# Optimization experiments

Hardware: AMD Instinct MI355X
Metric: run time of the kernel (lower is better)

The kernel has to match this reference:

```python
import jax, jax.numpy as jnp
import numpy as np

B, S, IN, E, L, H, NC, NL = 4, 1000, 5, 256, 6, 8, 2, 50
DH = E // H


def _ln(x, g, b, eps=1e-5):
    m = jnp.mean(x, -1, keepdims=True)
    v = jnp.mean((x - m) ** 2, -1, keepdims=True)
    return (x - m) / jnp.sqrt(v + eps) * g + b


def _lin(x, w, b):
    return x @ w.T + b


def _ph_single(points, fw, db, law, lab):
    # points: (S, 2) -> (6,) persistence features
    scores = (points @ law.T + lab)[:, 0]
    wts = jax.nn.softmax(scores)
    _, idx = jax.lax.top_k(wts, NL)
    lm = points[idx]  # (NL, 2) landmarks
    d2 = jnp.sum((lm[:, None, :] - lm[None, :, :]) ** 2, -1)
    # safe sqrt (zero grad on zero diagonal) == torch.cdist
    dist = jnp.sqrt(jnp.where(d2 > 0, d2, 1.0)) * (d2 > 0)
    sd = dist * jnp.abs(fw[0, 0]) + db[0]
    K = jnp.exp(-sd)
    lap = jnp.diag(jnp.sum(K, 1)) - K
    ev, evec = jnp.linalg.eigh(lap)
    zm = (ev < 1e-6).astype(ev.dtype)
    n0 = jnp.sum(zm)
    s0 = jnp.sum(jnp.abs(ev) * zm)
    gap = ev[1] - ev[0]
    fied = jnp.std(evec[:, 1], ddof=1)  # torch.std is unbiased
    return jnp.stack([n0, s0, gap, fied, jnp.mean(ev[2:6]), jnp.std(ev[2:6], ddof=1)])


def _attn(x, pf, qw, qb, kw, kb, vw, vb, pw1, pb1, pw2, pb2, ow_, ob_):
    b, s, e = x.shape
    q = _lin(x, qw, qb).reshape(b, s, H, DH).transpose(0, 2, 1, 3)
    k = _lin(x, kw, kb).reshape(b, s, H, DH).transpose(0, 2, 1, 3)
    v = _lin(x, vw, vb).reshape(b, s, H, DH).transpose(0, 2, 1, 3)
    scores = jnp.einsum('bhqd,bhkd->bhqk', q, k) / DH ** 0.5
    tw = jax.nn.sigmoid(_lin(jax.nn.relu(_lin(pf, pw1, pb1)), pw2, pb2))  # (b, E)
    # expand + mean over embed dim collapses to one scalar per sample
    ts = jnp.mean(tw, -1).reshape(b, 1, 1, 1)
    aw = jax.nn.softmax(scores * ts, -1)
    out = jnp.einsum('bhqk,bhkd->bhqd', aw, v).transpose(0, 2, 1, 3).reshape(b, s, e)
    return _lin(out, ow_, ob_)


def _fwd(sequences, ph_fw, ph_db, ph_law, ph_lab,
         emb_w1, emb_b1, emb_w2, emb_b2, emb_ln_g, emb_ln_b, pos_enc,
         qw, qb, kw, kb, vw, vb, pe_w1, pe_b1, pe_w2, pe_b2, ow, ob,
         ln_g, ln_b, f_w1, f_b1, f_w2, f_b2,
         c_ln_g, c_ln_b, c_w1, c_b1, c_w2, c_b2):
    b, s, _ = sequences.shape
    t = jnp.broadcast_to(jnp.arange(s, dtype=sequences.dtype), (b, s))
    pc = jnp.stack([t, jnp.mean(sequences, 2)], 2)  # (b, s, 2) point clouds
    pf = jax.vmap(lambda p: _ph_single(p, ph_fw, ph_db, ph_law, ph_lab))(pc)  # (b, 6)
    x = _ln(_lin(jax.nn.relu(_lin(sequences, emb_w1, emb_b1)), emb_w2, emb_b2),
            emb_ln_g, emb_ln_b)
    x = x + pos_enc[:s][None]
    for l in range(L):
        att = _attn(x, pf, qw[l], qb[l], kw[l], kb[l], vw[l], vb[l],
                    pe_w1[l], pe_b1[l], pe_w2[l], pe_b2[l], ow[l], ob[l])
        x = _ln(x + att, ln_g[l], ln_b[l])  # NOTE: same LN reused twice, as in source
        ff = _lin(jax.nn.gelu(_lin(x, f_w1[l], f_b1[l]), approximate=False), f_w2[l], f_b2[l])
        x = _ln(x + ff, ln_g[l], ln_b[l])
    pwts = jax.nn.softmax(jnp.sum(x, -1), -1)[..., None]
    pooled = jnp.sum(x * pwts, 1)
    z = jax.nn.relu(_lin(_ln(pooled, c_ln_g, c_ln_b), c_w1, c_b1))
    return _lin(z, c_w2, c_b2)


def setup_inputs() -> dict:
    key = jax.random.key(0)
    ks = iter(jax.random.split(key, 64))

    def w(shape, fan_in):
        return jax.random.normal(next(ks), shape, jnp.float32) / np.sqrt(fan_in).astype(np.float32)

    z = lambda *sh: jnp.zeros(sh, jnp.float32)
    o = lambda *sh: jnp.ones(sh, jnp.float32)
    return dict(
        sequences=jax.random.normal(next(ks), (B, S, IN), jnp.float32),
        ph_fw=jnp.full((1, 1), 0.02, jnp.float32),  # small filtration scale keeps eigh well-conditioned
        ph_db=z(1),
        ph_law=w((1, 2), 2), ph_lab=z(1),
        emb_w1=w((E // 2, IN), IN), emb_b1=z(E // 2),
        emb_w2=w((E, E // 2), E // 2), emb_b2=z(E),
        emb_ln_g=o(E), emb_ln_b=z(E),
        pos_enc=jax.random.normal(next(ks), (1000, E), jnp.float32),
        qw=w((L, E, E), E), qb=z(L, E),
        kw=w((L, E, E), E), kb=z(L, E),
        vw=w((L, E, E), E), vb=z(L, E),
        pe_w1=w((L, E // 2, 6), 6), pe_b1=z(L, E // 2),
        pe_w2=w((L, E, E // 2), E // 2), pe_b2=z(L, E),
        ow=w((L, E, E), E), ob=z(L, E),
        ln_g=o(L, E), ln_b=z(L, E),
        f_w1=w((L, 4 * E, E), E), f_b1=z(L, 4 * E),
        f_w2=w((L, E, 4 * E), 4 * E), f_b2=z(L, E),
        c_ln_g=o(E), c_ln_b=z(E),
        c_w1=w((E // 2, E), E), c_b1=z(E // 2),
        c_w2=w((NC, E // 2), E // 2), c_b2=z(NC),
    )


def reference(sequences, ph_fw, ph_db, ph_law, ph_lab,
              emb_w1, emb_b1, emb_w2, emb_b2, emb_ln_g, emb_ln_b, pos_enc,
              qw, qb, kw, kb, vw, vb, pe_w1, pe_b1, pe_w2, pe_b2, ow, ob,
              ln_g, ln_b, f_w1, f_b1, f_w2, f_b2,
              c_ln_g, c_ln_b, c_w1, c_b1, c_w2, c_b2):
    return _fwd(sequences, ph_fw, ph_db, ph_law, ph_lab,
                emb_w1, emb_b1, emb_w2, emb_b2, emb_ln_g, emb_ln_b, pos_enc,
                qw, qb, kw, kb, vw, vb, pe_w1, pe_b1, pe_w2, pe_b2, ow, ob,
                ln_g, ln_b, f_w1, f_b1, f_w2, f_b2,
                c_ln_g, c_ln_b, c_w1, c_b1, c_w2, c_b2)
```

## Files before the change

kernel.cpp:

```cpp
#include <hip/hip_runtime.h>
#include <math.h>

constexpr int BB = 4;
constexpr int SS = 1000;
constexpr int INDIM = 5;
constexpr int EE = 256;
constexpr int LL = 6;
constexpr int HH = 8;
constexpr int DHH = 32;
constexpr int NLM = 50;
constexpr int FFD = 1024;

typedef short short8 __attribute__((ext_vector_type(8)));
typedef float f32x4 __attribute__((ext_vector_type(4)));
typedef unsigned short u16;
typedef unsigned long long u64;

__device__ inline u16 f2b(float f) {
  union { float f; unsigned u; } v; v.f = f;
  unsigned u = v.u;
  unsigned r = u + 0x7FFFu + ((u >> 16) & 1u);
  return (u16)(r >> 16);
}
__device__ inline float b2f(u16 b) {
  union { unsigned u; float f; } v; v.u = ((unsigned)b) << 16;
  return v.f;
}
__device__ inline short8 pack8(float4 a, float4 b) {
  short8 r;
  r[0] = (short)f2b(a.x); r[1] = (short)f2b(a.y);
  r[2] = (short)f2b(a.z); r[3] = (short)f2b(a.w);
  r[4] = (short)f2b(b.x); r[5] = (short)f2b(b.y);
  r[6] = (short)f2b(b.z); r[7] = (short)f2b(b.w);
  return r;
}

__device__ inline double wred_sum(double v) {
#pragma unroll
  for (int m = 1; m < 64; m <<= 1) v += __shfl_xor(v, m, 64);
  return v;
}
__device__ inline double wred_min(double v) {
#pragma unroll
  for (int m = 1; m < 64; m <<= 1) v = fmin(v, __shfl_xor(v, m, 64));
  return v;
}
__device__ inline double wred_max(double v) {
#pragma unroll
  for (int m = 1; m < 64; m <<= 1) v = fmax(v, __shfl_xor(v, m, 64));
  return v;
}
__device__ inline float wredf_sum(float v) {
#pragma unroll
  for (int m = 1; m < 64; m <<= 1) v += __shfl_xor(v, m, 64);
  return v;
}
__device__ inline int sgnbit(double x) {
  return (int)((unsigned long long)__double_as_longlong(x) >> 63);
}

struct PhS {
  double matA[NLM][51];
  union {
    u64 keys[1024];
    double vstore[NLM - 2][64];
  } u;
  double vbuf[64], wbuf[64];
  double pm[4][64];
  double dar[NLM], ear[NLM], e2a[NLM], tauA[NLM], evs[NLM];
  double gdl[NLM], gdd[NLM], gdu[NLM], gdu2[NLM], gz[NLM];
  float sm[SS];
  float lx[NLM], ly[NLM];
};
union FusedS { PhS ph; float h[4][128]; };

__global__ __launch_bounds__(256) void phembed_kernel(
    const float* __restrict__ seq, const float* __restrict__ ph_fw,
    const float* __restrict__ ph_db, const float* __restrict__ ph_law,
    const float* __restrict__ ph_lab, float* __restrict__ pf,
    const float* __restrict__ ew1, const float* __restrict__ eb1,
    const float* __restrict__ ew2, const float* __restrict__ eb2,
    const float* __restrict__ eg, const float* __restrict__ ebe,
    const float* __restrict__ pos, float* __restrict__ X)
{
  __shared__ FusedS S;
  const int tid = threadIdx.x;
  const int lane = tid & 63, wid = tid >> 6;

  if (blockIdx.x < BB) {
    const int b = blockIdx.x;
    PhS& P = S.ph;
    const float law0 = ph_law[0], law1 = ph_law[1], labv = ph_lab[0];
    for (int s = tid; s < 1024; s += 256) {
      u64 key;
      if (s < SS) {
        const float* p = seq + ((size_t)b * SS + s) * INDIM;
        float m = (p[0] + p[1] + p[2] + p[3] + p[4]) * 0.2f;
        P.sm[s] = m;
        float sc = (float)s * law0 + m * law1 + labv;
        unsigned u = __float_as_uint(sc);
        unsigned asc = (u & 0x80000000u) ? ~u : (u | 0x80000000u);
        key = ((u64)(~asc) << 32) | (unsigned)s;
      } else {
        key = (0xFFFFFFFFull << 32) | (unsigned)s;
      }
      P.u.keys[s] = key;
    }
    __syncthreads();
    for (int k = 2; k <= 1024; k <<= 1) {
      for (int j = k >> 1; j > 0; j >>= 1) {
        for (int i = tid; i < 1024; i += 256) {
          int ixj = i ^ j;
          if (ixj > i) {
            u64 a = P.u.keys[i], c = P.u.keys[ixj];
            bool up = ((i & k) == 0);
            if ((a > c) == up) { P.u.keys[i] = c; P.u.keys[ixj] = a; }
          }
        }
        __syncthreads();
      }
    }
    if (tid < NLM) {
      int id = (int)(P.u.keys[tid] & 0xFFFFFFFFull);
      P.lx[tid] = (float)id;
      P.ly[tid] = P.sm[id];
    }
    __syncthreads();
    const float fwv = fabsf(ph_fw[0]);
    const float dbv = ph_db[0];
    for (int t = tid; t < NLM * NLM; t += 256) {
      int i = t / NLM, j = t % NLM;
      float dx = P.lx[i] - P.lx[j], dy = P.ly[i] - P.ly[j];
      float d2 = dx * dx + dy * dy;
      float dist = (d2 > 0.f) ? sqrtf(d2) : 0.f;
      float Kv = expf(-(dist * fwv + dbv));
      P.matA[i][j] = -(double)Kv;
    }
    __syncthreads();
    if (tid < NLM) {
      double rsum = 0.0;
      for (int j = 0; j < NLM; ++j) rsum -= P.matA[tid][j];
      P.matA[tid][tid] += rsum;
    }
    __syncthreads();

    for (int k = 0; k <= NLM - 3; ++k) {
      if (wid == 0) {
        double x = (lane > k && lane < NLM) ? P.matA[lane][k] : 0.0;
        double x0 = __shfl(x, k + 1, 64);
        double sigma = wred_sum((lane > k + 1) ? x * x : 0.0);
        double beta, tau, scale;
        if (sigma == 0.0) { beta = x0; tau = 0.0; scale = 0.0; }
        else {
          double nrm = sqrt(x0 * x0 + sigma);
          beta = (x0 >= 0.0) ? -nrm : nrm;
          tau = (beta - x0) / beta;
          scale = 1.0 / (x0 - beta);
        }
        double v = (lane == k + 1) ? 1.0 : ((lane > k + 1 && lane < NLM) ? x * scale : 0.0);
        P.vbuf[lane] = v;
        P.u.vstore[k][lane] = v;
        if (lane == 0) { P.ear[k] = beta; P.tauA[k] = tau; }
      }
      __syncthreads();
      {
        double partial = 0.0;
        if (lane < NLM) {
          int j0 = wid * 13;
#pragma unroll
          for (int jj = 0; jj < 13; ++jj) {
            int j = j0 + jj;
            if (j < NLM) partial += P.matA[lane][j] * P.vbuf[j];
          }
        }
        P.pm[wid][lane] = partial;
      }
      __syncthreads();
      if (wid == 0) {
        double tau = P.tauA[k];
        double p = 0.0;
        if (lane < NLM)
          p = (P.pm[0][lane] + P.pm[1][lane] + P.pm[2][lane] + P.pm[3][lane]) * tau;
        double vr = P.vbuf[lane];
        double dotvp = wred_sum(vr * p);
        double w = p - 0.5 * tau * dotvp * vr;
        P.wbuf[lane] = (lane < NLM) ? w : 0.0;
      }
      __syncthreads();
      if (lane < NLM) {
        double vr = P.vbuf[lane], wr = P.wbuf[lane];
        int j0 = wid * 13;
#pragma unroll
        for (int jj = 0; jj < 13; ++jj) {
          int j = j0 + jj;
          if (j < NLM) P.matA[lane][j] -= vr * P.wbuf[j] + wr * P.vbuf[j];
        }
      }
      __syncthreads();
    }
    if (tid < NLM) P.dar[tid] = P.matA[tid][tid];
    if (tid == 0) P.ear[NLM - 2] = P.matA[NLM - 1][NLM - 2];
    __syncthreads();
    if (tid < NLM - 1) P.e2a[tid] = P.ear[tid] * P.ear[tid];
    __syncthreads();

    double lo_i = 1e300, hi_i = -1e300;
    if (lane < NLM) {
      double rl = (lane > 0) ? fabs(P.ear[lane - 1]) : 0.0;
      double rr = (lane < NLM - 1) ? fabs(P.ear[lane]) : 0.0;
      double dd = P.dar[lane];
      lo_i = dd - rl - rr;
      hi_i = dd + rl + rr;
    }
    double glo = wred_min(lo_i), ghi = wred_max(hi_i);

    if (tid < 100) {
      const int e = tid >> 1;
      const int side = tid & 1;
      const int need = e + 1;
      double lo = glo, hi = ghi;
      for (int it = 0; it < 24; ++it) {
        double third = (hi - lo) * (1.0 / 3.0);
        double x1 = lo + third, x2 = hi - third;
        double x = side ? x2 : x1;
        double p = P.dar[0] - x, q = 1.0;
        int c = sgnbit(p);
#pragma unroll 7
        for (int i = 1; i < NLM; ++i) {
          double n = (P.dar[i] - x) * p - P.e2a[i - 1] * q;
          if (n == 0.0) n = sgnbit(p) ? -1e-300 : 1e-300;
          c += (sgnbit(n) != sgnbit(p));
          long long an = __double_as_longlong(n) & 0x7fffffffffffffffLL;
          long long ap = __double_as_longlong(p) & 0x7fffffffffffffffLL;
          int E = (int)((an > ap ? an : ap) >> 52);
          int se = 2046 - E; se = se < 1 ? 1 : (se > 2045 ? 2045 : se);
          double s = __longlong_as_double((long long)se << 52);
          q = p * s; p = n * s;
        }
        int cp = __shfl_xor(c, 1, 64);
        int c1 = side ? cp : c;
        int c2 = side ? c : cp;
        if (c1 >= need) hi = x1;
        else if (c2 >= need) { lo = x1; hi = x2; }
        else lo = x2;
      }
      if (side == 0) P.evs[e] = 0.5 * (lo + hi);
    }
    __syncthreads();

    if (wid != 0) return;

    if (lane == 0) {
      double shift = P.evs[1];
      unsigned rs = 12345u;
      for (int i = 0; i < NLM; ++i) {
        rs = rs * 1103515245u + 12345u;
        P.gz[i] = ((double)((rs >> 8) & 0xFFFF)) / 65536.0 - 0.5;
      }
      for (int iter = 0; iter < 2; ++iter) {
        for (int i = 0; i < NLM; ++i) P.gdd[i] = P.dar[i] - shift;
        for (int i = 0; i < NLM - 1; ++i) { P.gdl[i] = P.ear[i]; P.gdu[i] = P.ear[i]; }
        for (int i = 0; i < NLM - 1; ++i) {
          if (fabs(P.gdd[i]) >= fabs(P.gdl[i])) {
            if (P.gdd[i] == 0.0) P.gdd[i] = 1e-280;
            double fact = P.gdl[i] / P.gdd[i];
            P.gdd[i + 1] -= fact * P.gdu[i];
            P.gz[i + 1] -= fact * P.gz[i];
            if (i < NLM - 2) P.gdu2[i] = 0.0;
          } else {
            double fact = P.gdd[i] / P.gdl[i];
            P.gdd[i] = P.gdl[i];
            double tmp = P.gdd[i + 1];
            P.gdd[i + 1] = P.gdu[i] - fact * tmp;
            if (i < NLM - 2) { P.gdu2[i] = P.gdu[i + 1]; P.gdu[i + 1] = -fact * P.gdu2[i]; }
            P.gdu[i] = tmp;
            double tz = P.gz[i]; P.gz[i] = P.gz[i + 1]; P.gz[i + 1] = tz - fact * P.gz[i];
          }
        }
        if (P.gdd[NLM - 1] == 0.0) P.gdd[NLM - 1] = 1e-280;
        P.gz[NLM - 1] /= P.gdd[NLM - 1];
        P.gz[NLM - 2] = (P.gz[NLM - 2] - P.gdu[NLM - 2] * P.gz[NLM - 1]) / P.gdd[NLM - 2];
        for (int i = NLM - 3; i >= 0; --i)
          P.gz[i] = (P.gz[i] - P.gdu[i] * P.gz[i + 1] - P.gdu2[i] * P.gz[i + 2]) / P.gdd[i];
        double nr = 0.0;
        for (int i = 0; i < NLM; ++i) nr += P.gz[i] * P.gz[i];
        nr = sqrt(nr);
        for (int i = 0; i < NLM; ++i) P.gz[i] /= nr;
      }
    }
    __builtin_amdgcn_wave_barrier();
    double fied = (lane < NLM) ? P.gz[lane] : 0.0;
    for (int k = NLM - 3; k >= 0; --k) {
      double v = P.u.vstore[k][lane];
      double dot = wred_sum(v * fied);
      fied -= P.tauA[k] * dot * v;
    }

    double myev = (lane < NLM) ? P.evs[lane] : 1e300;
    bool inR = (lane < NLM);
    double n0 = wred_sum((inR && myev < 1e-6) ? 1.0 : 0.0);
    double s0 = wred_sum((inR && myev < 1e-6) ? fabs(myev) : 0.0);
    double e0 = P.evs[0], e1 = P.evs[1];
    double e2 = P.evs[2], e3 = P.evs[3], e4 = P.evs[4], e5 = P.evs[5];
    double gap = e1 - e0;
    double m4 = (e2 + e3 + e4 + e5) * 0.25;
    double v4 = ((e2 - m4) * (e2 - m4) + (e3 - m4) * (e3 - m4) +
                 (e4 - m4) * (e4 - m4) + (e5 - m4) * (e5 - m4)) / 3.0;
    double fmean = wred_sum(inR ? fied : 0.0) / NLM;
    double fd = inR ? (fied - fmean) : 0.0;
    double fvar = wred_sum(fd * fd) / (NLM - 1);
    if (lane == 0) {
      float* o = pf + b * 6;
      o[0] = (float)n0;
      o[1] = (float)s0;
      o[2] = (float)gap;
      o[3] = (float)sqrt(fvar);
      o[4] = (float)m4;
      o[5] = (float)sqrt(v4);
    }
    return;
  }

  const int row = (blockIdx.x - BB) * 4 + wid;
  const int s = row % SS;
  float* hb = S.h[wid];
  float sv0, sv1, sv2, sv3, sv4;
  {
    const float* p = seq + (size_t)row * INDIM;
    sv0 = p[0]; sv1 = p[1]; sv2 = p[2]; sv3 = p[3]; sv4 = p[4];
  }
#pragma unroll
  for (int half = 0; half < 2; ++half) {
    int j = lane + half * 64;
    const float* w = ew1 + j * INDIM;
    float a = eb1[j] + w[0] * sv0 + w[1] * sv1 + w[2] * sv2 + w[3] * sv3 + w[4] * sv4;
    hb[j] = fmaxf(a, 0.f);
  }
  __builtin_amdgcn_wave_barrier();
  float o4[4];
#pragma unroll
  for (int q = 0; q < 4; ++q) {
    int e = lane * 4 + q;
    const float* w = ew2 + (size_t)e * 128;
    float a0 = 0.f, a1 = 0.f;
    for (int i = 0; i < 128; i += 8) {
      float4 wa = *(const float4*)(w + i);
      float4 wb = *(const float4*)(w + i + 4);
      a0 += wa.x * hb[i] + wa.y * hb[i + 1] + wa.z * hb[i + 2] + wa.w * hb[i + 3];
      a1 += wb.x * hb[i + 4] + wb.y * hb[i + 5] + wb.z * hb[i + 6] + wb.w * hb[i + 7];
    }
    o4[q] = eb2[e] + a0 + a1;
  }
  float ssum = o4[0] + o4[1] + o4[2] + o4[3];
  ssum = wredf_sum(ssum);
  float mean = ssum * (1.f / EE);
  float d0 = o4[0] - mean, d1 = o4[1] - mean, d2 = o4[2] - mean, d3 = o4[3] - mean;
  float qsum = d0 * d0 + d1 * d1 + d2 * d2 + d3 * d3;
  qsum = wredf_sum(qsum);
  float inv = rsqrtf(qsum * (1.f / EE) + 1e-5f);
  float4 gv = *(const float4*)(eg + lane * 4);
  float4 bv = *(const float4*)(ebe + lane * 4);
  float4 pv = *(const float4*)(pos + (size_t)s * EE + lane * 4);
  float4 outv = make_float4(d0 * inv * gv.x + bv.x + pv.x,
                            d1 * inv * gv.y + bv.y + pv.y,
                            d2 * inv * gv.z + bv.z + pv.z,
                            d3 * inv * gv.w + bv.w + pv.w);
  *(float4*)(X + (size_t)row * EE + lane * 4) = outv;
}

__global__ __launch_bounds__(256) void temp_kernel(
    const float* __restrict__ pf, const float* __restrict__ w1, const float* __restrict__ b1,
    const float* __restrict__ w2, const float* __restrict__ b2, float* __restrict__ ts)
{
  const int l = blockIdx.x / BB, b = blockIdx.x % BB, tid = threadIdx.x;
  __shared__ float pfl[6];
  __shared__ float h[128];
  __shared__ float red[256];
  if (tid < 6) pfl[tid] = pf[b * 6 + tid];
  __syncthreads();
  if (tid < 128) {
    const float* w = w1 + ((size_t)l * 128 + tid) * 6;
    float a = b1[(size_t)l * 128 + tid];
#pragma unroll
    for (int i = 0; i < 6; ++i) a += w[i] * pfl[i];
    h[tid] = fmaxf(a, 0.f);
  }
  __syncthreads();
  const float* w = w2 + ((size_t)l * EE + tid) * 128;
  float a = b2[(size_t)l * EE + tid];
  for (int i = 0; i < 128; ++i) a += w[i] * h[i];
  float sg = 1.f / (1.f + expf(-a));
  red[tid] = sg; __syncthreads();
  for (int wd = 128; wd > 0; wd >>= 1) { if (tid < wd) red[tid] += red[tid + wd]; __syncthreads(); }
  if (tid == 0) ts[l * BB + b] = red[0] * (1.f / EE);
}

template <int AF32, int ACT>
__global__ __launch_bounds__(256) void gemm_bt(
    const void* __restrict__ Aptr,
    const float* __restrict__ W0, const float* __restrict__ W1, const float* __restrict__ W2,
    const float* __restrict__ bb0, const float* __restrict__ bb1, const float* __restrict__ bb2,
    u16* __restrict__ C0, u16* __restrict__ C1, u16* __restrict__ C2,
    int M, int N, int K)
{
  const int z = blockIdx.z;
  const float* W = (z == 0) ? W0 : (z == 1) ? W1 : W2;
  const float* bias = (z == 0) ? bb0 : (z == 1) ? bb1 : bb2;
  u16* C = (z == 0) ? C0 : (z == 1) ? C1 : C2;
  __shared__ __align__(16) u16 As[2][64][40];
  __shared__ __align__(16) u16 Bs[2][64][40];
  const int m0 = blockIdx.x * 64, n0 = blockIdx.y * 64;
  const int tid = threadIdx.x;
  const int lane = tid & 63, wave = tid >> 6;
  const int wm = wave >> 1, wn = wave & 1;
  const int l15 = lane & 15, l4 = lane >> 4;
  const int srow = tid >> 2, scg = (tid & 3) * 8;

  const float* Af = (const float*)Aptr;
  const u16* Ab = (const u16*)Aptr;

  f32x4 acc[2][2];
#pragma unroll
  for (int i = 0; i < 2; ++i)
#pragma unroll
    for (int j = 0; j < 2; ++j) acc[i][j] = (f32x4){0.f, 0.f, 0.f, 0.f};

  short8 areg, breg;
  auto do_load = [&](int t) {
    int kk = t * 32 + scg;
    if (AF32) {
      float4 a0 = *(const float4*)(Af + (size_t)(m0 + srow) * K + kk);
      float4 a1 = *(const float4*)(Af + (size_t)(m0 + srow) * K + kk + 4);
      areg = pack8(a0, a1);
    } else {
      areg = *(const short8*)(Ab + (size_t)(m0 + srow) * K + kk);
    }
    float4 b0 = *(const float4*)(W + (size_t)(n0 + srow) * K + kk);
    float4 b1 = *(const float4*)(W + (size_t)(n0 + srow) * K + kk + 4);
    breg = pack8(b0, b1);
  };
  auto do_write = [&](int buf) {
    *(short8*)&As[buf][srow][scg] = areg;
    *(short8*)&Bs[buf][srow][scg] = breg;
  };

  const int NT = K / 32;
  do_load(0);
  do_write(0);
  __syncthreads();
  for (int t = 0; t < NT; ++t) {
    const int cur = t & 1;
    if (t + 1 < NT) do_load(t + 1);
    short8 af0 = *(const short8*)&As[cur][wm * 32 + l15][l4 * 8];
    short8 af1 = *(const short8*)&As[cur][wm * 32 + 16 + l15][l4 * 8];
    short8 bf0 = *(const short8*)&Bs[cur][wn * 32 + l15][l4 * 8];
    short8 bf1 = *(const short8*)&Bs[cur][wn * 32 + 16 + l15][l4 * 8];
    acc[0][0] = __builtin_amdgcn_mfma_f32_16x16x32_bf16(af0, bf0, acc[0][0], 0, 0, 0);
    acc[0][1] = __builtin_amdgcn_mfma_f32_16x16x32_bf16(af0, bf1, acc[0][1], 0, 0, 0);
    acc[1][0] = __builtin_amdgcn_mfma_f32_16x16x32_bf16(af1, bf0, acc[1][0], 0, 0, 0);
    acc[1][1] = __builtin_amdgcn_mfma_f32_16x16x32_bf16(af1, bf1, acc[1][1], 0, 0, 0);
    if (t + 1 < NT) do_write(cur ^ 1);
    __syncthreads();
  }
#pragma unroll
  for (int nf = 0; nf < 2; ++nf) {
    int col = n0 + wn * 32 + nf * 16 + l15;
    float bv = bias[col];
#pragma unroll
    for (int mf = 0; mf < 2; ++mf) {
#pragma unroll
      for (int r = 0; r < 4; ++r) {
        int row = m0 + wm * 32 + mf * 16 + l4 * 4 + r;
        if (row < M) {
          float v = acc[mf][nf][r] + bv;
          if (ACT == 1) v = 0.5f * v * (1.f + erff(v * 0.70710678118654752440f));
          C[(size_t)row * N + col] = f2b(v);
        }
      }
    }
  }
}

__global__ __launch_bounds__(256) void attn_mfma(
    const u16* __restrict__ Qm, const u16* __restrict__ Km, const u16* __restrict__ Vm,
    const float* __restrict__ ts, u16* __restrict__ Om, int l)
{
  const int qt = blockIdx.x, h = blockIdx.y, b = blockIdx.z;
  const int tid = threadIdx.x;
  const int lane = tid & 63, wave = tid >> 6;
  const int l15 = lane & 15, l4 = lane >> 4;
  const float scale = ts[l * BB + b] * 0.17677669529663688110f;
  __shared__ __align__(16) u16 Ks[64][40];
  __shared__ __align__(16) u16 Vt[32][72];
  __shared__ __align__(16) u16 Pw[4][16][72];
  const int q0 = qt * 64 + wave * 16;
  const int srow = tid >> 2, scg = (tid & 3) * 8;

  short8 qf = {0, 0, 0, 0, 0, 0, 0, 0};
  {
    int qrow = q0 + l15;
    if (qrow < SS)
      qf = *(const short8*)(Qm + ((size_t)(b * SS + qrow)) * EE + h * DHH + l4 * 8);
  }

  float mrun[4] = {-INFINITY, -INFINITY, -INFINITY, -INFINITY};
  float lrun[4] = {0.f, 0.f, 0.f, 0.f};
  f32x4 Oacc[2];
  Oacc[0] = (f32x4){0.f, 0.f, 0.f, 0.f};
  Oacc[1] = (f32x4){0.f, 0.f, 0.f, 0.f};

  for (int k0 = 0; k0 < SS; k0 += 64) {
    int kn = SS - k0; if (kn > 64) kn = 64;
    __syncthreads();
    {
      short8 kv8 = {0, 0, 0, 0, 0, 0, 0, 0};
      if (srow < kn)
        kv8 = *(const short8*)(Km + ((size_t)(b * SS + k0 + srow)) * EE + h * DHH + scg);
      *(short8*)&Ks[srow][scg] = kv8;
    }
    {
      int d = tid & 31, kb = tid >> 5;
      u16 uu[8];
#pragma unroll
      for (int i = 0; i < 8; ++i) {
        int kv = kb * 8 + i;
        uu[i] = (kv < kn) ? Vm[((size_t)(b * SS + k0 + kv)) * EE + h * DHH + d] : (u16)0;
      }
      *(ushort4*)(&Vt[d][kb * 8])     = make_ushort4(uu[0], uu[1], uu[2], uu[3]);
      *(ushort4*)(&Vt[d][kb * 8 + 4]) = make_ushort4(uu[4], uu[5], uu[6], uu[7]);
    }
    __syncthreads();

    f32x4 sa[4];
#pragma unroll
    for (int nf = 0; nf < 4; ++nf) {
      short8 kf = *(const short8*)(&Ks[nf * 16 + l15][l4 * 8]);
      f32x4 zz = (f32x4){0.f, 0.f, 0.f, 0.f};
      sa[nf] = __builtin_amdgcn_mfma_f32_16x16x32_bf16(qf, kf, zz, 0, 0, 0);
    }
#pragma unroll
    for (int nf = 0; nf < 4; ++nf) {
      bool valid = (nf * 16 + l15) < kn;
#pragma unroll
      for (int r = 0; r < 4; ++r)
        sa[nf][r] = valid ? sa[nf][r] * scale : -INFINITY;
    }
    float pv[4][4];
#pragma unroll
    for (int r = 0; r < 4; ++r) {
      float tmax = fmaxf(fmaxf(sa[0][r], sa[1][r]), fmaxf(sa[2][r], sa[3][r]));
#pragma unroll
      for (int m = 1; m < 16; m <<= 1) tmax = fmaxf(tmax, __shfl_xor(tmax, m, 64));
      float mnew = fmaxf(mrun[r], tmax);
      float fac = expf(mrun[r] - mnew);
      float rsum = 0.f;
#pragma unroll
      for (int nf = 0; nf < 4; ++nf) {
        float p = expf(sa[nf][r] - mnew);
        pv[nf][r] = p;
        rsum += p;
      }
#pragma unroll
      for (int m = 1; m < 16; m <<= 1) rsum += __shfl_xor(rsum, m, 64);
      lrun[r] = lrun[r] * fac + rsum;
      mrun[r] = mnew;
      Oacc[0][r] *= fac;
      Oacc[1][r] *= fac;
    }
#pragma unroll
    for (int nf = 0; nf < 4; ++nf)
#pragma unroll
      for (int r = 0; r < 4; ++r)
        Pw[wave][l4 * 4 + r][nf * 16 + l15] = f2b(pv[nf][r]);
    asm volatile("s_waitcnt lgkmcnt(0)" ::: "memory");
    __builtin_amdgcn_sched_barrier(0);
#pragma unroll
    for (int ka = 0; ka < 2; ++ka) {
      short8 pa = *(const short8*)(&Pw[wave][l15][ka * 32 + l4 * 8]);
#pragma unroll
      for (int df = 0; df < 2; ++df) {
        short8 vf = *(const short8*)(&Vt[df * 16 + l15][ka * 32 + l4 * 8]);
        Oacc[df] = __builtin_amdgcn_mfma_f32_16x16x32_bf16(pa, vf, Oacc[df], 0, 0, 0);
      }
    }
  }
#pragma unroll
  for (int df = 0; df < 2; ++df)
#pragma unroll
    for (int r = 0; r < 4; ++r) {
      int qrow = q0 + l4 * 4 + r;
      if (qrow < SS)
        Om[((size_t)(b * SS + qrow)) * EE + h * DHH + df * 16 + l15] = f2b(Oacc[df][r] / lrun[r]);
    }
}

__global__ __launch_bounds__(256) void addln_kernel(
    float* __restrict__ X, const u16* __restrict__ T,
    const float* __restrict__ g, const float* __restrict__ be)
{
  const int row = blockIdx.x * 4 + (threadIdx.x >> 6);
  const int lane = threadIdx.x & 63;
  float4 xv = *(float4*)(X + (size_t)row * EE + lane * 4);
  ushort4 tv = *(const ushort4*)(T + (size_t)row * EE + lane * 4);
  float4 v = make_float4(xv.x + b2f(tv.x), xv.y + b2f(tv.y),
                         xv.z + b2f(tv.z), xv.w + b2f(tv.w));
  float s = v.x + v.y + v.z + v.w;
  s = wredf_sum(s);
  float mean = s * (1.f / EE);
  float4 d = make_float4(v.x - mean, v.y - mean, v.z - mean, v.w - mean);
  float q = d.x * d.x + d.y * d.y + d.z * d.z + d.w * d.w;
  q = wredf_sum(q);
  float inv = rsqrtf(q * (1.f / EE) + 1e-5f);
  float4 gv = *(const float4*)(g + lane * 4);
  float4 bv = *(const float4*)(be + lane * 4);
  float4 o = make_float4(d.x * inv * gv.x + bv.x, d.y * inv * gv.y + bv.y,
                         d.z * inv * gv.z + bv.z, d.w * inv * gv.w + bv.w);
  *(float4*)(X + (size_t)row * EE + lane * 4) = o;
}

__global__ __launch_bounds__(256) void final_kernel(
    const float* __restrict__ X, const float* __restrict__ g, const float* __restrict__ be,
    const float* __restrict__ w1, const float* __restrict__ b1,
    const float* __restrict__ w2, const float* __restrict__ b2,
    float* __restrict__ out)
{
  const int b = blockIdx.x, tid = threadIdx.x;
  __shared__ float rs[SS];
  __shared__ float red[256];
  __shared__ float pooled[EE];
  __shared__ float h[128];
  for (int s = tid; s < SS; s += 256) {
    const float* xr = X + ((size_t)(b * SS + s)) * EE;
    float a = 0.f;
    for (int e = 0; e < EE; ++e) a += xr[e];
    rs[s] = a;
  }
  __syncthreads();
  float mx = -INFINITY;
  for (int s = tid; s < SS; s += 256) mx = fmaxf(mx, rs[s]);
  red[tid] = mx; __syncthreads();
  for (int w = 128; w > 0; w >>= 1) { if (tid < w) red[tid] = fmaxf(red[tid], red[tid + w]); __syncthreads(); }
  mx = red[0]; __syncthreads();
  float sme = 0.f;
  for (int s = tid; s < SS; s += 256) { float e2 = expf(rs[s] - mx); rs[s] = e2; sme += e2; }
  red[tid] = sme; __syncthreads();
  for (int w = 128; w > 0; w >>= 1) { if (tid < w) red[tid] += red[tid + w]; __syncthreads(); }
  float tot = red[0]; __syncthreads();
  float acc = 0.f;
  for (int s = 0; s < SS; ++s) acc += X[((size_t)(b * SS + s)) * EE + tid] * rs[s];
  acc /= tot;
  red[tid] = acc; __syncthreads();
  for (int w = 128; w > 0; w >>= 1) { if (tid < w) red[tid] += red[tid + w]; __syncthreads(); }
  float mean = red[0] * (1.f / EE); __syncthreads();
  float d = acc - mean;
  red[tid] = d * d; __syncthreads();
  for (int w = 128; w > 0; w >>= 1) { if (tid < w) red[tid] += red[tid + w]; __syncthreads(); }
  float var = red[0] * (1.f / EE);
  pooled[tid] = d * rsqrtf(var + 1e-5f) * g[tid] + be[tid];
  __syncthreads();
  if (tid < 128) {
    const float* w = w1 + (size_t)tid * EE;
    float a = b1[tid];
    for (int e = 0; e < EE; ++e) a += w[e] * pooled[e];
    h[tid] = fmaxf(a, 0.f);
  }
  __syncthreads();
  if (tid < 2) {
    const float* w = w2 + (size_t)tid * 128;
    float a = b2[tid];
    for (int j = 0; j < 128; ++j) a += w[j] * h[j];
    out[b * 2 + tid] = a;
  }
}

extern "C" void kernel_launch(void* const* d_in, const int* in_sizes, int n_in,
                              void* d_out, int out_size, void* d_ws, size_t ws_size,
                              hipStream_t stream) {
  (void)in_sizes; (void)n_in; (void)out_size; (void)ws_size;
  const float* seq    = (const float*)d_in[0];
  const float* ph_fw  = (const float*)d_in[1];
  const float* ph_db  = (const float*)d_in[2];
  const float* ph_law = (const float*)d_in[3];
  const float* ph_lab = (const float*)d_in[4];
  const float* emb_w1 = (const float*)d_in[5];
  const float* emb_b1 = (const float*)d_in[6];
  const float* emb_w2 = (const float*)d_in[7];
  const float* emb_b2 = (const float*)d_in[8];
  const float* eln_g  = (const float*)d_in[9];
  const float* eln_b  = (const float*)d_in[10];
  const float* pos    = (const float*)d_in[11];
  const float* qw     = (const float*)d_in[12];
  const float* qb     = (const float*)d_in[13];
  const float* kw     = (const float*)d_in[14];
  const float* kb     = (const float*)d_in[15];
  const float* vw     = (const float*)d_in[16];
  const float* vb     = (const float*)d_in[17];
  const float* pw1    = (const float*)d_in[18];
  const float* pb1    = (const float*)d_in[19];
  const float* pw2    = (const float*)d_in[20];
  const float* pb2    = (const float*)d_in[21];
  const float* ow     = (const float*)d_in[22];
  const float* obv    = (const float*)d_in[23];
  const float* lng    = (const float*)d_in[24];
  const float* lnb    = (const float*)d_in[25];
  const float* fw1    = (const float*)d_in[26];
  const float* fb1    = (const float*)d_in[27];
  const float* fw2    = (const float*)d_in[28];
  const float* fb2    = (const float*)d_in[29];
  const float* clng   = (const float*)d_in[30];
  const float* clnb   = (const float*)d_in[31];
  const float* cw1    = (const float*)d_in[32];
  const float* cb1    = (const float*)d_in[33];
  const float* cw2    = (const float*)d_in[34];
  const float* cb2    = (const float*)d_in[35];

  float* ws  = (float*)d_ws;
  float* pf  = ws;
  float* tsv = ws + 32;
  const size_t SL = (size_t)4096 * 256;
  float* X = ws + 256;
  u16* Qb   = (u16*)(X + SL);
  u16* Kb   = Qb + SL;
  u16* Vb   = Kb + SL;
  u16* ATTb = Vb + SL;
  u16* TMPb = ATTb + SL;
  u16* HIDb = TMPb + SL;
  const int M = BB * SS;

  phembed_kernel<<<BB + M / 4, 256, 0, stream>>>(
      seq, ph_fw, ph_db, ph_law, ph_lab, pf,
      emb_w1, emb_b1, emb_w2, emb_b2, eln_g, eln_b, pos, X);
  temp_kernel<<<LL * BB, 256, 0, stream>>>(pf, pw1, pb1, pw2, pb2, tsv);

  const int GM = 63;
  for (int l = 0; l < LL; ++l) {
    const size_t wo = (size_t)l * EE * EE;
    gemm_bt<1, 0><<<dim3(GM, EE / 64, 3), 256, 0, stream>>>(
        X, qw + wo, kw + wo, vw + wo, qb + l * EE, kb + l * EE, vb + l * EE,
        Qb, Kb, Vb, M, EE, EE);
    attn_mfma<<<dim3(16, HH, BB), 256, 0, stream>>>(Qb, Kb, Vb, tsv, ATTb, l);
    gemm_bt<0, 0><<<dim3(GM, EE / 64, 1), 256, 0, stream>>>(
        ATTb, ow + wo, ow + wo, ow + wo, obv + l * EE, obv + l * EE, obv + l * EE,
        TMPb, TMPb, TMPb, M, EE, EE);
    addln_kernel<<<M / 4, 256, 0, stream>>>(X, TMPb, lng + l * EE, lnb + l * EE);
    gemm_bt<1, 1><<<dim3(GM, FFD / 64, 1), 256, 0, stream>>>(
        X, fw1 + (size_t)l * FFD * EE, fw1 + (size_t)l * FFD * EE, fw1 + (size_t)l * FFD * EE,
        fb1 + (size_t)l * FFD, fb1 + (size_t)l * FFD, fb1 + (size_t)l * FFD,
        HIDb, HIDb, HIDb, M, FFD, EE);
    gemm_bt<0, 0><<<dim3(GM, EE / 64, 1), 256, 0, stream>>>(
        HIDb, fw2 + (size_t)l * EE * FFD, fw2 + (size_t)l * EE * FFD, fw2 + (size_t)l * EE * FFD,
        fb2 + l * EE, fb2 + l * EE, fb2 + l * EE,
        TMPb, TMPb, TMPb, M, EE, FFD);
    addln_kernel<<<M / 4, 256, 0, stream>>>(X, TMPb, lng + l * EE, lnb + l * EE);
  }

  final_kernel<<<BB, 256, 0, stream>>>(X, clng, clnb, cw1, cb1, cw2, cb2, (float*)d_out);
}
```

Before: 979.4 us.

## Fuse output projections with residual add and LayerNorm, keep bf16 activation copy

Adds a gemm_ln16 kernel in which each block computes a 16-row by full-256-column tile, so the residual add and LayerNorm can run in its epilogue. This replaces the separate gemm plus addln pairs for the attention output and FFN second projections. The embedding and LN epilogues also write a bf16 copy of X, so the QKV and FFN1 GEMMs read bf16 instead of converting fp32 on load. The cost is that the fused kernel converts fp32 weights to bf16 per block with 250 blocks, which repeats weight traffic, and it computes variance as E[x^2]-mean^2.

```diff
diff --git a/kernel.cpp b/kernel.cpp
--- a/kernel.cpp
+++ b/kernel.cpp
@@ -81,7 +81,7 @@
     const float* __restrict__ ew1, const float* __restrict__ eb1,
     const float* __restrict__ ew2, const float* __restrict__ eb2,
     const float* __restrict__ eg, const float* __restrict__ ebe,
-    const float* __restrict__ pos, float* __restrict__ X)
+    const float* __restrict__ pos, float* __restrict__ X, u16* __restrict__ Xb)
 {
   __shared__ FusedS S;
   const int tid = threadIdx.x;
@@ -366,6 +366,8 @@
                             d2 * inv * gv.z + bv.z + pv.z,
                             d3 * inv * gv.w + bv.w + pv.w);
   *(float4*)(X + (size_t)row * EE + lane * 4) = outv;
+  *(ushort4*)(Xb + (size_t)row * EE + lane * 4) =
+      make_ushort4(f2b(outv.x), f2b(outv.y), f2b(outv.z), f2b(outv.w));
 }
 
 __global__ __launch_bounds__(256) void temp_kernel(
@@ -481,6 +483,109 @@
   }
 }
 
+template <int K>
+__global__ __launch_bounds__(256) void gemm_ln16(
+    const u16* __restrict__ A, const float* __restrict__ W,
+    const float* __restrict__ bias, const float* __restrict__ g,
+    const float* __restrict__ be, float* __restrict__ X, u16* __restrict__ Xb)
+{
+  __shared__ __align__(16) u16 As[2][16][40];
+  __shared__ __align__(16) u16 Bs[2][256][40];
+  __shared__ float wsum[4][16], wsq[4][16];
+  const int m0 = blockIdx.x * 16;
+  const int tid = threadIdx.x;
+  const int lane = tid & 63, wave = tid >> 6;
+  const int l15 = lane & 15, l4 = lane >> 4;
+
+  f32x4 acc[4];
+#pragma unroll
+  for (int i = 0; i < 4; ++i) acc[i] = (f32x4){0.f, 0.f, 0.f, 0.f};
+
+  short8 areg, breg[4];
+  auto do_load = [&](int t) {
+    int kk = t * 32;
+    if (tid < 64) {
+      int arow = tid >> 2, acg = (tid & 3) * 8;
+      areg = *(const short8*)(A + (size_t)(m0 + arow) * K + kk + acg);
+    }
+#pragma unroll
+    for (int q = 0; q < 4; ++q) {
+      float4 b0 = *(const float4*)(W + (size_t)tid * K + kk + q * 8);
+      float4 b1 = *(const float4*)(W + (size_t)tid * K + kk + q * 8 + 4);
+      breg[q] = pack8(b0, b1);
+    }
+  };
+  auto do_write = [&](int buf) {
+    if (tid < 64) {
+      int arow = tid >> 2, acg = (tid & 3) * 8;
+      *(short8*)&As[buf][arow][acg] = areg;
+    }
+#pragma unroll
+    for (int q = 0; q < 4; ++q) *(short8*)&Bs[buf][tid][q * 8] = breg[q];
+  };
+
+  const int NT = K / 32;
+  do_load(0);
+  do_write(0);
+  __syncthreads();
+  for (int t = 0; t < NT; ++t) {
+    const int cur = t & 1;
+    if (t + 1 < NT) do_load(t + 1);
+    short8 af = *(const short8*)&As[cur][l15][l4 * 8];
+#pragma unroll
+    for (int nf = 0; nf < 4; ++nf) {
+      short8 bf = *(const short8*)&Bs[cur][wave * 64 + nf * 16 + l15][l4 * 8];
+      acc[nf] = __builtin_amdgcn_mfma_f32_16x16x32_bf16(af, bf, acc[nf], 0, 0, 0);
+    }
+    if (t + 1 < NT) do_write(cur ^ 1);
+    __syncthreads();
+  }
+
+#pragma unroll
+  for (int nf = 0; nf < 4; ++nf) {
+    int col = wave * 64 + nf * 16 + l15;
+    float bv = bias[col];
+#pragma unroll
+    for (int r = 0; r < 4; ++r) {
+      int row = m0 + l4 * 4 + r;
+      acc[nf][r] += bv + X[(size_t)row * EE + col];
+    }
+  }
+#pragma unroll
+  for (int r = 0; r < 4; ++r) {
+    float s = acc[0][r] + acc[1][r] + acc[2][r] + acc[3][r];
+    float q = acc[0][r] * acc[0][r] + acc[1][r] * acc[1][r] +
+              acc[2][r] * acc[2][r] + acc[3][r] * acc[3][r];
+#pragma unroll
+    for (int m = 1; m < 16; m <<= 1) {
+      s += __shfl_xor(s, m, 64);
+      q += __shfl_xor(q, m, 64);
+    }
+    if (l15 == 0) {
+      wsum[wave][l4 * 4 + r] = s;
+      wsq[wave][l4 * 4 + r] = q;
+    }
+  }
+  __syncthreads();
+#pragma unroll
+  for (int r = 0; r < 4; ++r) {
+    int rl = l4 * 4 + r;
+    float Ssum = wsum[0][rl] + wsum[1][rl] + wsum[2][rl] + wsum[3][rl];
+    float Qsum = wsq[0][rl] + wsq[1][rl] + wsq[2][rl] + wsq[3][rl];
+    float mean = Ssum * (1.f / EE);
+    float var = Qsum * (1.f / EE) - mean * mean;
+    float inv = rsqrtf(var + 1e-5f);
+    int row = m0 + rl;
+#pragma unroll
+    for (int nf = 0; nf < 4; ++nf) {
+      int col = wave * 64 + nf * 16 + l15;
+      float o = (acc[nf][r] - mean) * inv * g[col] + be[col];
+      X[(size_t)row * EE + col] = o;
+      Xb[(size_t)row * EE + col] = f2b(o);
+    }
+  }
+}
+
 __global__ __launch_bounds__(256) void attn_mfma(
     const u16* __restrict__ Qm, const u16* __restrict__ Km, const u16* __restrict__ Vm,
     const float* __restrict__ ts, u16* __restrict__ Om, int l)
@@ -592,30 +697,6 @@
       if (qrow < SS)
         Om[((size_t)(b * SS + qrow)) * EE + h * DHH + df * 16 + l15] = f2b(Oacc[df][r] / lrun[r]);
     }
-}
-
-__global__ __launch_bounds__(256) void addln_kernel(
-    float* __restrict__ X, const u16* __restrict__ T,
-    const float* __restrict__ g, const float* __restrict__ be)
-{
-  const int row = blockIdx.x * 4 + (threadIdx.x >> 6);
-  const int lane = threadIdx.x & 63;
-  float4 xv = *(float4*)(X + (size_t)row * EE + lane * 4);
-  ushort4 tv = *(const ushort4*)(T + (size_t)row * EE + lane * 4);
-  float4 v = make_float4(xv.x + b2f(tv.x), xv.y + b2f(tv.y),
-                         xv.z + b2f(tv.z), xv.w + b2f(tv.w));
-  float s = v.x + v.y + v.z + v.w;
-  s = wredf_sum(s);
-  float mean = s * (1.f / EE);
-  float4 d = make_float4(v.x - mean, v.y - mean, v.z - mean, v.w - mean);
-  float q = d.x * d.x + d.y * d.y + d.z * d.z + d.w * d.w;
-  q = wredf_sum(q);
-  float inv = rsqrtf(q * (1.f / EE) + 1e-5f);
-  float4 gv = *(const float4*)(g + lane * 4);
-  float4 bv = *(const float4*)(be + lane * 4);
-  float4 o = make_float4(d.x * inv * gv.x + bv.x, d.y * inv * gv.y + bv.y,
-                         d.z * inv * gv.z + bv.z, d.w * inv * gv.w + bv.w);
-  *(float4*)(X + (size_t)row * EE + lane * 4) = o;
 }
 
 __global__ __launch_bounds__(256) void final_kernel(
@@ -719,39 +800,35 @@
   float* tsv = ws + 32;
   const size_t SL = (size_t)4096 * 256;
   float* X = ws + 256;
-  u16* Qb   = (u16*)(X + SL);
+  u16* Xb   = (u16*)(X + SL);
+  u16* Qb   = Xb + SL;
   u16* Kb   = Qb + SL;
   u16* Vb   = Kb + SL;
   u16* ATTb = Vb + SL;
-  u16* TMPb = ATTb + SL;
-  u16* HIDb = TMPb + SL;
+  u16* HIDb = ATTb + SL;
   const int M = BB * SS;
 
   phembed_kernel<<<BB + M / 4, 256, 0, stream>>>(
       seq, ph_fw, ph_db, ph_law, ph_lab, pf,
-      emb_w1, emb_b1, emb_w2, emb_b2, eln_g, eln_b, pos, X);
+      emb_w1, emb_b1, emb_w2, emb_b2, eln_g, eln_b, pos, X, Xb);
   temp_kernel<<<LL * BB, 256, 0, stream>>>(pf, pw1, pb1, pw2, pb2, tsv);
 
   const int GM = 63;
+  const int GL = 250;
   for (int l = 0; l < LL; ++l) {
     const size_t wo = (size_t)l * EE * EE;
-    gemm_bt<1, 0><<<dim3(GM, EE / 64, 3), 256, 0, stream>>>(
-        X, qw + wo, kw + wo, vw + wo, qb + l * EE, kb + l * EE, vb + l * EE,
+    gemm_bt<0, 0><<<dim3(GM, EE / 64, 3), 256, 0, stream>>>(
+        Xb, qw + wo, kw + wo, vw + wo, qb + l * EE, kb + l * EE, vb + l * EE,
         Qb, Kb, Vb, M, EE, EE);
     attn_mfma<<<dim3(16, HH, BB), 256, 0, stream>>>(Qb, Kb, Vb, tsv, ATTb, l);
-    gemm_bt<0, 0><<<dim3(GM, EE / 64, 1), 256, 0, stream>>>(
-        ATTb, ow + wo, ow + wo, ow + wo, obv + l * EE, obv + l * EE, obv + l * EE,
-        TMPb, TMPb, TMPb, M, EE, EE);
-    addln_kernel<<<M / 4, 256, 0, stream>>>(X, TMPb, lng + l * EE, lnb + l * EE);
-    gemm_bt<1, 1><<<dim3(GM, FFD / 64, 1), 256, 0, stream>>>(
-        X, fw1 + (size_t)l * FFD * EE, fw1 + (size_t)l * FFD * EE, fw1 + (size_t)l * FFD * EE,
+    gemm_ln16<EE><<<GL, 256, 0, stream>>>(
+        ATTb, ow + wo, obv + l * EE, lng + l * EE, lnb + l * EE, X, Xb);
+    gemm_bt<0, 1><<<dim3(GM, FFD / 64, 1), 256, 0, stream>>>(
+        Xb, fw1 + (size_t)l * FFD * EE, fw1 + (size_t)l * FFD * EE, fw1 + (size_t)l * FFD * EE,
         fb1 + (size_t)l * FFD, fb1 + (size_t)l * FFD, fb1 + (size_t)l * FFD,
         HIDb, HIDb, HIDb, M, FFD, EE);
-    gemm_bt<0, 0><<<dim3(GM, EE / 64, 1), 256, 0, stream>>>(
-        HIDb, fw2 + (size_t)l * EE * FFD, fw2 + (size_t)l * EE * FFD, fw2 + (size_t)l * EE * FFD,
-        fb2 + l * EE, fb2 + l * EE, fb2 + l * EE,
-        TMPb, TMPb, TMPb, M, EE, FFD);
-    addln_kernel<<<M / 4, 256, 0, stream>>>(X, TMPb, lng + l * EE, lnb + l * EE);
+    gemm_ln16<FFD><<<GL, 256, 0, stream>>>(
+        HIDb, fw2 + (size_t)l * EE * FFD, fb2 + l * EE, lng + l * EE, lnb + l * EE, X, Xb);
   }
 
   final_kernel<<<BB, 256, 0, stream>>>(X, clng, clnb, cw1, cb1, cw2, cb2, (float*)d_out);
```

Measured after the change: 1.140 ms. 16.4% more time.
